# Kernel tuning notes

Measured on AMD Instinct MI355X. Metric: run time of the kernel, lower is better.

The kernel has to match this reference:

```python
import jax, jax.numpy as jnp
import numpy as np

TOP_K = 4  # num_experts_per_tok


def setup_inputs() -> dict:
    key = jax.random.key(0)
    ks = jax.random.split(key, 7)
    B, S, H, E, I = 1, 1024, 1024, 16, 2880
    scale_h = 1.0 / np.sqrt(H)
    scale_i = 1.0 / np.sqrt(I)
    return {
        "hidden_states": jax.random.normal(ks[0], (B, S, H), jnp.float32),
        "gate_w": jax.random.normal(ks[1], (E, H), jnp.float32) * scale_h,
        "gate_b": jax.random.normal(ks[2], (E,), jnp.float32) * 0.01,
        "gate_up_proj": jax.random.normal(ks[3], (E, H, 2 * I), jnp.float32) * scale_h,
        "gate_up_proj_bias": jax.random.normal(ks[4], (E, 2 * I), jnp.float32) * 0.01,
        "down_proj": jax.random.normal(ks[5], (E, I, H), jnp.float32) * scale_i,
        "down_proj_bias": jax.random.normal(ks[6], (E, H), jnp.float32) * 0.01,
    }


def reference(hidden_states, gate_w, gate_b, gate_up_proj, gate_up_proj_bias,
              down_proj, down_proj_bias):
    B, S, H = hidden_states.shape
    E = gate_w.shape[0]
    I = down_proj.shape[1]
    x = hidden_states.reshape(-1, H)  # [T, H]
    T = x.shape[0]

    # Router: top-k logits, softmax over selected logits only
    router_logits = x @ gate_w.T + gate_b          # [T, E]
    top_vals, top_idx = jax.lax.top_k(router_logits, TOP_K)
    routing_weights = jax.nn.softmax(top_vals, axis=-1)  # [T, K]

    # Combine matrix: C[t, e] = routing weight of expert e for token t (0 if unselected)
    C = jnp.zeros((T, E), x.dtype).at[jnp.arange(T)[:, None], top_idx].add(routing_weights)

    # Dense per-expert MLP (reference computes all experts, combine masks unselected)
    gu = jnp.einsum('th,ehf->tef', x, gate_up_proj) + gate_up_proj_bias[None]  # [T, E, 2I]
    gate, up = gu[..., :I], gu[..., I:]
    inter = jax.nn.silu(gate) * up                                            # [T, E, I]
    expert_out = jnp.einsum('tei,eih->teh', inter, down_proj) + down_proj_bias[None]  # [T, E, H]
    out = jnp.einsum('teh,te->th', expert_out, C)                             # [T, H]

    return out.reshape(B, S, H), router_logits
```

## Files before the change

kernel.cpp:

```cpp
#include <hip/hip_runtime.h>
#include <hip/hip_bf16.h>
#include <stdint.h>

#define T_TOK 1024
#define HDIM  1024
#define NEXP  16
#define IDIM  2880
#define GU_COLS (2*IDIM)
#define TOPK  4

using short4v  = __attribute__((ext_vector_type(4))) short;
using short8   = __attribute__((ext_vector_type(8))) short;
using ushort4v = __attribute__((ext_vector_type(4))) unsigned short;
using f32x4    = __attribute__((ext_vector_type(4))) float;

__device__ __forceinline__ unsigned short f2b(float f) {
    union { float f; unsigned u; } x; x.f = f;
    unsigned r = x.u + 0x7FFFu + ((x.u >> 16) & 1u);
    return (unsigned short)(r >> 16);
}

typedef const __attribute__((address_space(1))) unsigned int* gas1_t;
typedef __attribute__((address_space(3))) unsigned int* las3_t;
__device__ __forceinline__ void gload16(const void* g, void* l) {
    __builtin_amdgcn_global_load_lds((gas1_t)g, (las3_t)l, 16, 0, 0);
}

__global__ __launch_bounds__(256) void router_kernel(
    const float* __restrict__ x, const float* __restrict__ gw,
    const float* __restrict__ gb, float* __restrict__ logits_out,
    int* __restrict__ counts, int* __restrict__ lists, float* __restrict__ wts,
    int* __restrict__ tokslot4, float* __restrict__ wts4,
    unsigned short* __restrict__ xb)
{
    int t = blockIdx.x;
    int tid = threadIdx.x;
    const float* xr = x + (size_t)t * HDIM;
    {
        float4 v = *(const float4*)(xr + tid * 4);
        ushort4v b; b.x = f2b(v.x); b.y = f2b(v.y); b.z = f2b(v.z); b.w = f2b(v.w);
        *(ushort4v*)(xb + (size_t)t * HDIM + tid * 4) = b;
    }
    int e = tid >> 4;
    int l16 = tid & 15;
    const float* wr = gw + (size_t)e * HDIM;
    float p = 0.f;
    for (int h = l16; h < HDIM; h += 16) p += xr[h] * wr[h];
    p += __shfl_xor(p, 8);
    p += __shfl_xor(p, 4);
    p += __shfl_xor(p, 2);
    p += __shfl_xor(p, 1);
    __shared__ float sl[NEXP];
    if (l16 == 0) {
        float v = p + gb[e];
        sl[e] = v;
        logits_out[t * NEXP + e] = v;
    }
    __syncthreads();
    if (tid == 0) {
        float v[NEXP];
#pragma unroll
        for (int i = 0; i < NEXP; ++i) v[i] = sl[i];
        int idx[TOPK]; float tv[TOPK];
        unsigned used = 0;
#pragma unroll
        for (int k = 0; k < TOPK; ++k) {
            float best = -__builtin_inff(); int bi = 0;
#pragma unroll
            for (int i = 0; i < NEXP; ++i)
                if (!((used >> i) & 1u) && v[i] > best) { best = v[i]; bi = i; }
            used |= 1u << bi; idx[k] = bi; tv[k] = best;
        }
        float m = tv[0];
        float ex[TOPK], s = 0.f;
#pragma unroll
        for (int k = 0; k < TOPK; ++k) { ex[k] = expf(tv[k] - m); s += ex[k]; }
#pragma unroll
        for (int k = 0; k < TOPK; ++k) {
            float w = ex[k] / s;
            int slot = atomicAdd(&counts[idx[k]], 1);
            lists[idx[k] * T_TOK + slot] = t;
            wts[idx[k] * T_TOK + slot] = w;
            tokslot4[t * TOPK + k] = (idx[k] << 16) | slot;
            wts4[t * TOPK + k] = w;
        }
    }
}

__global__ void offsets_kernel(const int* __restrict__ counts, int* __restrict__ offsets)
{
    if (threadIdx.x == 0) {
        int o = 0;
        for (int e = 0; e < NEXP; ++e) { offsets[e] = o; o += counts[e]; }
        offsets[NEXP] = o;
    }
}

__global__ __launch_bounds__(512) void gu_kernel(
    const unsigned short* __restrict__ xb, const float* __restrict__ gup,
    const float* __restrict__ gub, const int* __restrict__ counts,
    const int* __restrict__ offsets, const int* __restrict__ lists,
    unsigned short* __restrict__ inter)
{
    int bid = blockIdx.x;
    int xcd = bid & 7;
    int r   = bid >> 3;
    int nt  = r % 90;
    int s   = r / 90;
    int e   = xcd + ((s & 1) << 3);
    int mt  = s >> 1;
    int ne = counts[e];
    if (mt * 256 >= ne) return;

    int tid = threadIdx.x;
    int wave = tid >> 6, lane = tid & 63;
    int l16 = lane & 15, lq = lane >> 4;

    __shared__ int tokid[256];
    __shared__ unsigned short As[256 * 64];
    __shared__ unsigned short Bs[64 * 64];

    if (tid < 256) {
        int slot = mt * 256 + tid;
        tokid[tid] = (slot < ne) ? lists[e * T_TOK + slot] : lists[e * T_TOK];
    }
    __syncthreads();

    const float* gup_e = gup + (size_t)e * HDIM * GU_COLS;

    int at = tid - 256;
    const unsigned short* asrc[8];
    if (tid >= 256) {
#pragma unroll
        for (int i = 0; i < 8; ++i) {
            int s2 = at + i * 256;
            int row = s2 >> 3, c = s2 & 7;
            asrc[i] = xb + (size_t)tokid[row] * HDIM + ((c ^ (row & 7)) * 8);
        }
    }
    int nb = tid & 15, kb = tid >> 4;
    const float* bsrc = nullptr;
    if (tid < 256) {
        int n0 = nb * 4;
        size_t col = (n0 < 32) ? (size_t)(nt * 32 + n0) : (size_t)(IDIM + nt * 32 + (n0 - 32));
        bsrc = gup_e + (size_t)(kb * 4) * GU_COLS + col;
    }

    f32x4 acc[2][4];
#pragma unroll
    for (int i = 0; i < 2; ++i)
#pragma unroll
        for (int f = 0; f < 4; ++f) acc[i][f] = (f32x4){0.f, 0.f, 0.f, 0.f};

    float4 br0, br1, br2, br3;
    if (tid < 256) {
        br0 = *(const float4*)(bsrc);
        br1 = *(const float4*)(bsrc + GU_COLS);
        br2 = *(const float4*)(bsrc + 2 * GU_COLS);
        br3 = *(const float4*)(bsrc + 3 * GU_COLS);
    }

    for (int kk = 0; kk < HDIM; kk += 64) {
        __syncthreads();
        if (tid >= 256) {
#pragma unroll
            for (int i = 0; i < 8; ++i)
                gload16(asrc[i] + kk, As + ((size_t)(at + i * 256)) * 8);
        } else {
#pragma unroll
            for (int j = 0; j < 4; ++j) {
                int n = nb * 4 + j;
                int slot = kb ^ (n & 15);
                ushort4v b;
                b.x = f2b((&br0.x)[j]); b.y = f2b((&br1.x)[j]);
                b.z = f2b((&br2.x)[j]); b.w = f2b((&br3.x)[j]);
                *(ushort4v*)&Bs[n * 64 + slot * 4] = b;
            }
        }
        __syncthreads();
        if (tid < 256 && kk + 64 < HDIM) {
            const float* sp = bsrc + (size_t)(kk + 64) * GU_COLS;
            br0 = *(const float4*)(sp);
            br1 = *(const float4*)(sp + GU_COLS);
            br2 = *(const float4*)(sp + 2 * GU_COLS);
            br3 = *(const float4*)(sp + 3 * GU_COLS);
        }
        __builtin_amdgcn_s_setprio(1);
#pragma unroll
        for (int ks = 0; ks < 2; ++ks) {
            short8 a[2], b[4];
#pragma unroll
            for (int i = 0; i < 2; ++i) {
                int row = wave * 32 + i * 16 + l16;
                int q = ks * 4 + lq;
                a[i] = *(const short8*)&As[row * 64 + ((q ^ (row & 7)) * 8)];
            }
#pragma unroll
            for (int f = 0; f < 4; ++f) {
                int n = f * 16 + l16;
                int u0 = (ks * 8 + lq * 2) ^ (n & 15);
                int u1 = (ks * 8 + lq * 2 + 1) ^ (n & 15);
                short4v h0 = *(const short4v*)&Bs[n * 64 + u0 * 4];
                short4v h1 = *(const short4v*)&Bs[n * 64 + u1 * 4];
                b[f] = __builtin_shufflevector(h0, h1, 0, 1, 2, 3, 4, 5, 6, 7);
            }
#pragma unroll
            for (int i = 0; i < 2; ++i)
#pragma unroll
                for (int f = 0; f < 4; ++f)
                    acc[i][f] = __builtin_amdgcn_mfma_f32_16x16x32_bf16(a[i], b[f], acc[i][f], 0, 0, 0);
        }
        __builtin_amdgcn_s_setprio(0);
    }

    int off = offsets[e];
    const float* gbe = gub + (size_t)e * GU_COLS;
#pragma unroll
    for (int j = 0; j < 2; ++j) {
        int col = j * 16 + l16;
        float bg = gbe[nt * 32 + col];
        float bu = gbe[IDIM + nt * 32 + col];
#pragma unroll
        for (int i = 0; i < 2; ++i)
#pragma unroll
            for (int r2 = 0; r2 < 4; ++r2) {
                int row = wave * 32 + i * 16 + lq * 4 + r2;
                int slot = mt * 256 + row;
                if (slot < ne) {
                    float g = acc[i][j][r2] + bg;
                    float u = acc[i][j + 2][r2] + bu;
                    float sg = g / (1.f + expf(-g));
                    inter[(size_t)(off + slot) * IDIM + nt * 32 + col] = f2b(sg * u);
                }
            }
    }
}

__global__ __launch_bounds__(512) void down_kernel(
    const unsigned short* __restrict__ inter, const float* __restrict__ dw,
    const float* __restrict__ db, const int* __restrict__ counts,
    const int* __restrict__ offsets, float* __restrict__ eo)
{
    int bid = blockIdx.x;
    int xcd = bid & 7;
    int r   = bid >> 3;
    int ht  = r & 15;
    int s   = r >> 4;
    int e   = xcd + ((s & 1) << 3);
    int mt  = s >> 1;
    int ne = counts[e];
    if (mt * 256 >= ne) return;

    int tid = threadIdx.x;
    int wave = tid >> 6, lane = tid & 63;
    int l16 = lane & 15, lq = lane >> 4;

    __shared__ unsigned short As[256 * 64];
    __shared__ unsigned short Bs[64 * 64];

    int off = offsets[e];

    const float* dw_e = dw + (size_t)e * IDIM * HDIM;

    int at = tid - 256;
    const unsigned short* asrc[8];
    if (tid >= 256) {
#pragma unroll
        for (int i = 0; i < 8; ++i) {
            int s2 = at + i * 256;
            int row = s2 >> 3, c = s2 & 7;
            int slotr = mt * 256 + row; if (slotr >= ne) slotr = ne - 1;
            asrc[i] = inter + (size_t)(off + slotr) * IDIM + ((c ^ (row & 7)) * 8);
        }
    }
    int nb = tid & 15, kb = tid >> 4;
    const float* bsrc = nullptr;
    if (tid < 256)
        bsrc = dw_e + (size_t)(kb * 4) * HDIM + ht * 64 + nb * 4;

    f32x4 acc[2][4];
#pragma unroll
    for (int i = 0; i < 2; ++i)
#pragma unroll
        for (int f = 0; f < 4; ++f) acc[i][f] = (f32x4){0.f, 0.f, 0.f, 0.f};

    float4 br0, br1, br2, br3;
    if (tid < 256) {
        br0 = *(const float4*)(bsrc);
        br1 = *(const float4*)(bsrc + HDIM);
        br2 = *(const float4*)(bsrc + 2 * HDIM);
        br3 = *(const float4*)(bsrc + 3 * HDIM);
    }

    for (int kk = 0; kk < IDIM; kk += 64) {
        __syncthreads();
        if (tid >= 256) {
#pragma unroll
            for (int i = 0; i < 8; ++i)
                gload16(asrc[i] + kk, As + ((size_t)(at + i * 256)) * 8);
        } else {
#pragma unroll
            for (int j = 0; j < 4; ++j) {
                int n = nb * 4 + j;
                int slot = kb ^ (n & 15);
                ushort4v b;
                b.x = f2b((&br0.x)[j]); b.y = f2b((&br1.x)[j]);
                b.z = f2b((&br2.x)[j]); b.w = f2b((&br3.x)[j]);
                *(ushort4v*)&Bs[n * 64 + slot * 4] = b;
            }
        }
        __syncthreads();
        if (tid < 256 && kk + 64 < IDIM) {
            const float* sp = bsrc + (size_t)(kk + 64) * HDIM;
            br0 = *(const float4*)(sp);
            br1 = *(const float4*)(sp + HDIM);
            br2 = *(const float4*)(sp + 2 * HDIM);
            br3 = *(const float4*)(sp + 3 * HDIM);
        }
        __builtin_amdgcn_s_setprio(1);
#pragma unroll
        for (int ks = 0; ks < 2; ++ks) {
            short8 a[2], b[4];
#pragma unroll
            for (int i = 0; i < 2; ++i) {
                int row = wave * 32 + i * 16 + l16;
                int q = ks * 4 + lq;
                a[i] = *(const short8*)&As[row * 64 + ((q ^ (row & 7)) * 8)];
            }
#pragma unroll
            for (int f = 0; f < 4; ++f) {
                int n = f * 16 + l16;
                int u0 = (ks * 8 + lq * 2) ^ (n & 15);
                int u1 = (ks * 8 + lq * 2 + 1) ^ (n & 15);
                short4v h0 = *(const short4v*)&Bs[n * 64 + u0 * 4];
                short4v h1 = *(const short4v*)&Bs[n * 64 + u1 * 4];
                b[f] = __builtin_shufflevector(h0, h1, 0, 1, 2, 3, 4, 5, 6, 7);
            }
#pragma unroll
            for (int i = 0; i < 2; ++i)
#pragma unroll
                for (int f = 0; f < 4; ++f)
                    acc[i][f] = __builtin_amdgcn_mfma_f32_16x16x32_bf16(a[i], b[f], acc[i][f], 0, 0, 0);
        }
        __builtin_amdgcn_s_setprio(0);
    }

    const float* db_e = db + (size_t)e * HDIM;
#pragma unroll
    for (int f = 0; f < 4; ++f) {
        int h = ht * 64 + f * 16 + l16;
        float bias = db_e[h];
#pragma unroll
        for (int i = 0; i < 2; ++i)
#pragma unroll
            for (int r2 = 0; r2 < 4; ++r2) {
                int row = wave * 32 + i * 16 + lq * 4 + r2;
                int slot = mt * 256 + row;
                if (slot < ne)
                    eo[(size_t)(off + slot) * HDIM + h] = acc[i][f][r2] + bias;
            }
    }
}

__global__ __launch_bounds__(256) void gather_kernel(
    const float* __restrict__ eo, const int* __restrict__ tokslot4,
    const float* __restrict__ wts4, const int* __restrict__ offsets,
    float* __restrict__ out)
{
    int t = blockIdx.x;
    int tid = threadIdx.x;
    int rows[TOPK]; float w[TOPK];
#pragma unroll
    for (int k = 0; k < TOPK; ++k) {
        int ts = tokslot4[t * TOPK + k];
        int e = ts >> 16, slot = ts & 0xFFFF;
        rows[k] = offsets[e] + slot;
        w[k] = wts4[t * TOPK + k];
    }
    int h0 = tid * 4;
    float4 s = make_float4(0.f, 0.f, 0.f, 0.f);
#pragma unroll
    for (int k = 0; k < TOPK; ++k) {
        float4 v = *(const float4*)(eo + (size_t)rows[k] * HDIM + h0);
        s.x += w[k] * v.x; s.y += w[k] * v.y;
        s.z += w[k] * v.z; s.w += w[k] * v.w;
    }
    *(float4*)(out + (size_t)t * HDIM + h0) = s;
}

extern "C" void kernel_launch(void* const* d_in, const int* in_sizes, int n_in,
                              void* d_out, int out_size, void* d_ws, size_t ws_size,
                              hipStream_t stream)
{
    const float* x   = (const float*)d_in[0];
    const float* gw  = (const float*)d_in[1];
    const float* gb  = (const float*)d_in[2];
    const float* gup = (const float*)d_in[3];
    const float* gub = (const float*)d_in[4];
    const float* dw  = (const float*)d_in[5];
    const float* db  = (const float*)d_in[6];

    float* out        = (float*)d_out;
    float* logits_out = out + (size_t)T_TOK * HDIM;

    char* ws = (char*)d_ws;
    int*   counts   = (int*)(ws + 0);
    int*   offsets  = (int*)(ws + 256);
    int*   lists    = (int*)(ws + 512);
    float* wts      = (float*)(ws + 512 + 65536);
    int*   tokslot4 = (int*)(ws + 512 + 131072);
    float* wts4     = (float*)(ws + 512 + 131072 + 16384);
    unsigned short* xb    = (unsigned short*)(ws + 164352);
    unsigned short* inter = (unsigned short*)(ws + 2261504);
    float*          eo    = (float*)(ws + 25854464);

    hipMemsetAsync(counts, 0, 64, stream);

    router_kernel<<<T_TOK, 256, 0, stream>>>(x, gw, gb, logits_out, counts, lists, wts, tokslot4, wts4, xb);
    offsets_kernel<<<1, 64, 0, stream>>>(counts, offsets);
    gu_kernel<<<8 * 90 * 8, 512, 0, stream>>>(xb, gup, gub, counts, offsets, lists, inter);
    down_kernel<<<8 * 16 * 8, 512, 0, stream>>>(inter, dw, db, counts, offsets, eo);
    gather_kernel<<<T_TOK, 256, 0, stream>>>(eo, tokslot4, wts4, offsets, out);
}
```

Before: 303.7 us.

## Double-buffer LDS tiles in gate-up and down GEMMs with async prefetch

```diff
diff --git a/kernel.cpp b/kernel.cpp
--- a/kernel.cpp
+++ b/kernel.cpp
@@ -115,32 +115,28 @@
     int tid = threadIdx.x;
     int wave = tid >> 6, lane = tid & 63;
     int l16 = lane & 15, lq = lane >> 4;
-
-    __shared__ int tokid[256];
-    __shared__ unsigned short As[256 * 64];
-    __shared__ unsigned short Bs[64 * 64];
-
-    if (tid < 256) {
-        int slot = mt * 256 + tid;
-        tokid[tid] = (slot < ne) ? lists[e * T_TOK + slot] : lists[e * T_TOK];
-    }
-    __syncthreads();
+    bool a_wave = (tid >= 256);
+
+    __shared__ unsigned short As[2 * 256 * 64];
+    __shared__ unsigned short Bs[2 * 64 * 64];
 
     const float* gup_e = gup + (size_t)e * HDIM * GU_COLS;
 
     int at = tid - 256;
     const unsigned short* asrc[8];
-    if (tid >= 256) {
+    if (a_wave) {
 #pragma unroll
         for (int i = 0; i < 8; ++i) {
             int s2 = at + i * 256;
             int row = s2 >> 3, c = s2 & 7;
-            asrc[i] = xb + (size_t)tokid[row] * HDIM + ((c ^ (row & 7)) * 8);
+            int slot = mt * 256 + row;
+            int tok = lists[e * T_TOK + (slot < ne ? slot : 0)];
+            asrc[i] = xb + (size_t)tok * HDIM + ((c ^ (row & 7)) * 8);
         }
     }
     int nb = tid & 15, kb = tid >> 4;
     const float* bsrc = nullptr;
-    if (tid < 256) {
+    if (!a_wave) {
         int n0 = nb * 4;
         size_t col = (n0 < 32) ? (size_t)(nt * 32 + n0) : (size_t)(IDIM + nt * 32 + (n0 - 32));
         bsrc = gup_e + (size_t)(kb * 4) * GU_COLS + col;
@@ -153,38 +149,69 @@
         for (int f = 0; f < 4; ++f) acc[i][f] = (f32x4){0.f, 0.f, 0.f, 0.f};
 
     float4 br0, br1, br2, br3;
-    if (tid < 256) {
+    if (a_wave) {
+#pragma unroll
+        for (int i = 0; i < 8; ++i)
+            gload16(asrc[i], As + ((size_t)(at + i * 256)) * 8);
+    } else {
         br0 = *(const float4*)(bsrc);
         br1 = *(const float4*)(bsrc + GU_COLS);
         br2 = *(const float4*)(bsrc + 2 * GU_COLS);
         br3 = *(const float4*)(bsrc + 3 * GU_COLS);
-    }
-
-    for (int kk = 0; kk < HDIM; kk += 64) {
-        __syncthreads();
-        if (tid >= 256) {
-#pragma unroll
-            for (int i = 0; i < 8; ++i)
-                gload16(asrc[i] + kk, As + ((size_t)(at + i * 256)) * 8);
+#pragma unroll
+        for (int j = 0; j < 4; ++j) {
+            int n = nb * 4 + j;
+            int slot = kb ^ (n & 15);
+            ushort4v b;
+            b.x = f2b((&br0.x)[j]); b.y = f2b((&br1.x)[j]);
+            b.z = f2b((&br2.x)[j]); b.w = f2b((&br3.x)[j]);
+            *(ushort4v*)&Bs[n * 64 + slot * 4] = b;
+        }
+        const float* sp = bsrc + (size_t)64 * GU_COLS;
+        br0 = *(const float4*)(sp);
+        br1 = *(const float4*)(sp + GU_COLS);
+        br2 = *(const float4*)(sp + 2 * GU_COLS);
+        br3 = *(const float4*)(sp + 3 * GU_COLS);
+    }
+    __syncthreads();
+
+    const int NP = HDIM / 64;
+    for (int p = 0; p < NP; ++p) {
+        int cur = p & 1, nxt = cur ^ 1;
+        __builtin_amdgcn_s_barrier();
+        __builtin_amdgcn_sched_barrier(0);
+        if (p + 1 < NP) {
+            if (a_wave) {
+#pragma unroll
+                for (int i = 0; i < 8; ++i)
+                    gload16(asrc[i] + (p + 1) * 64, As + (size_t)nxt * 16384 + ((size_t)(at + i * 256)) * 8);
+            } else {
+#pragma unroll
+                for (int j = 0; j < 4; ++j) {
+                    int n = nb * 4 + j;
+                    int slot = kb ^ (n & 15);
+                    ushort4v b;
+                    b.x = f2b((&br0.x)[j]); b.y = f2b((&br1.x)[j]);
+                    b.z = f2b((&br2.x)[j]); b.w = f2b((&br3.x)[j]);
+                    *(ushort4v*)&Bs[nxt * 4096 + n * 64 + slot * 4] = b;
+                }
+                if (p + 2 < NP) {
+                    const float* sp = bsrc + (size_t)(p + 2) * 64 * GU_COLS;
+                    br0 = *(const float4*)(sp);
+                    br1 = *(const float4*)(sp + GU_COLS);
+                    br2 = *(const float4*)(sp + 2 * GU_COLS);
+                    br3 = *(const float4*)(sp + 3 * GU_COLS);
+                }
+            }
+        }
+        if (a_wave) {
+            if (p + 1 < NP) asm volatile("s_waitcnt vmcnt(8)" ::: "memory");
+            else            asm volatile("s_waitcnt vmcnt(0)" ::: "memory");
         } else {
-#pragma unroll
-            for (int j = 0; j < 4; ++j) {
-                int n = nb * 4 + j;
-                int slot = kb ^ (n & 15);
-                ushort4v b;
-                b.x = f2b((&br0.x)[j]); b.y = f2b((&br1.x)[j]);
-                b.z = f2b((&br2.x)[j]); b.w = f2b((&br3.x)[j]);
-                *(ushort4v*)&Bs[n * 64 + slot * 4] = b;
-            }
-        }
-        __syncthreads();
-        if (tid < 256 && kk + 64 < HDIM) {
-            const float* sp = bsrc + (size_t)(kk + 64) * GU_COLS;
-            br0 = *(const float4*)(sp);
-            br1 = *(const float4*)(sp + GU_COLS);
-            br2 = *(const float4*)(sp + 2 * GU_COLS);
-            br3 = *(const float4*)(sp + 3 * GU_COLS);
-        }
+            asm volatile("s_waitcnt lgkmcnt(0)" ::: "memory");
+        }
+        __builtin_amdgcn_s_barrier();
+        __builtin_amdgcn_sched_barrier(0);
         __builtin_amdgcn_s_setprio(1);
 #pragma unroll
         for (int ks = 0; ks < 2; ++ks) {
@@ -193,15 +220,15 @@
             for (int i = 0; i < 2; ++i) {
                 int row = wave * 32 + i * 16 + l16;
                 int q = ks * 4 + lq;
-                a[i] = *(const short8*)&As[row * 64 + ((q ^ (row & 7)) * 8)];
+                a[i] = *(const short8*)&As[cur * 16384 + row * 64 + ((q ^ (row & 7)) * 8)];
             }
 #pragma unroll
             for (int f = 0; f < 4; ++f) {
                 int n = f * 16 + l16;
                 int u0 = (ks * 8 + lq * 2) ^ (n & 15);
                 int u1 = (ks * 8 + lq * 2 + 1) ^ (n & 15);
-                short4v h0 = *(const short4v*)&Bs[n * 64 + u0 * 4];
-                short4v h1 = *(const short4v*)&Bs[n * 64 + u1 * 4];
+                short4v h0 = *(const short4v*)&Bs[cur * 4096 + n * 64 + u0 * 4];
+                short4v h1 = *(const short4v*)&Bs[cur * 4096 + n * 64 + u1 * 4];
                 b[f] = __builtin_shufflevector(h0, h1, 0, 1, 2, 3, 4, 5, 6, 7);
             }
 #pragma unroll
@@ -254,17 +281,17 @@
     int tid = threadIdx.x;
     int wave = tid >> 6, lane = tid & 63;
     int l16 = lane & 15, lq = lane >> 4;
-
-    __shared__ unsigned short As[256 * 64];
-    __shared__ unsigned short Bs[64 * 64];
+    bool a_wave = (tid >= 256);
+
+    __shared__ unsigned short As[2 * 256 * 64];
+    __shared__ unsigned short Bs[2 * 64 * 64];
 
     int off = offsets[e];
-
     const float* dw_e = dw + (size_t)e * IDIM * HDIM;
 
     int at = tid - 256;
     const unsigned short* asrc[8];
-    if (tid >= 256) {
+    if (a_wave) {
 #pragma unroll
         for (int i = 0; i < 8; ++i) {
             int s2 = at + i * 256;
@@ -275,7 +302,7 @@
     }
     int nb = tid & 15, kb = tid >> 4;
     const float* bsrc = nullptr;
-    if (tid < 256)
+    if (!a_wave)
         bsrc = dw_e + (size_t)(kb * 4) * HDIM + ht * 64 + nb * 4;
 
     f32x4 acc[2][4];
@@ -285,38 +312,69 @@
         for (int f = 0; f < 4; ++f) acc[i][f] = (f32x4){0.f, 0.f, 0.f, 0.f};
 
     float4 br0, br1, br2, br3;
-    if (tid < 256) {
+    if (a_wave) {
+#pragma unroll
+        for (int i = 0; i < 8; ++i)
+            gload16(asrc[i], As + ((size_t)(at + i * 256)) * 8);
+    } else {
         br0 = *(const float4*)(bsrc);
         br1 = *(const float4*)(bsrc + HDIM);
         br2 = *(const float4*)(bsrc + 2 * HDIM);
         br3 = *(const float4*)(bsrc + 3 * HDIM);
-    }
-
-    for (int kk = 0; kk < IDIM; kk += 64) {
-        __syncthreads();
-        if (tid >= 256) {
-#pragma unroll
-            for (int i = 0; i < 8; ++i)
-                gload16(asrc[i] + kk, As + ((size_t)(at + i * 256)) * 8);
+#pragma unroll
+        for (int j = 0; j < 4; ++j) {
+            int n = nb * 4 + j;
+            int slot = kb ^ (n & 15);
+            ushort4v b;
+            b.x = f2b((&br0.x)[j]); b.y = f2b((&br1.x)[j]);
+            b.z = f2b((&br2.x)[j]); b.w = f2b((&br3.x)[j]);
+            *(ushort4v*)&Bs[n * 64 + slot * 4] = b;
+        }
+        const float* sp = bsrc + (size_t)64 * HDIM;
+        br0 = *(const float4*)(sp);
+        br1 = *(const float4*)(sp + HDIM);
+        br2 = *(const float4*)(sp + 2 * HDIM);
+        br3 = *(const float4*)(sp + 3 * HDIM);
+    }
+    __syncthreads();
+
+    const int NP = IDIM / 64;
+    for (int p = 0; p < NP; ++p) {
+        int cur = p & 1, nxt = cur ^ 1;
+        __builtin_amdgcn_s_barrier();
+        __builtin_amdgcn_sched_barrier(0);
+        if (p + 1 < NP) {
+            if (a_wave) {
+#pragma unroll
+                for (int i = 0; i < 8; ++i)
+                    gload16(asrc[i] + (p + 1) * 64, As + (size_t)nxt * 16384 + ((size_t)(at + i * 256)) * 8);
+            } else {
+#pragma unroll
+                for (int j = 0; j < 4; ++j) {
+                    int n = nb * 4 + j;
+                    int slot = kb ^ (n & 15);
+                    ushort4v b;
+                    b.x = f2b((&br0.x)[j]); b.y = f2b((&br1.x)[j]);
+                    b.z = f2b((&br2.x)[j]); b.w = f2b((&br3.x)[j]);
+                    *(ushort4v*)&Bs[nxt * 4096 + n * 64 + slot * 4] = b;
+                }
+                if (p + 2 < NP) {
+                    const float* sp = bsrc + (size_t)(p + 2) * 64 * HDIM;
+                    br0 = *(const float4*)(sp);
+                    br1 = *(const float4*)(sp + HDIM);
+                    br2 = *(const float4*)(sp + 2 * HDIM);
+                    br3 = *(const float4*)(sp + 3 * HDIM);
+                }
+            }
+        }
+        if (a_wave) {
+            if (p + 1 < NP) asm volatile("s_waitcnt vmcnt(8)" ::: "memory");
+            else            asm volatile("s_waitcnt vmcnt(0)" ::: "memory");
         } else {
-#pragma unroll
-            for (int j = 0; j < 4; ++j) {
-                int n = nb * 4 + j;
-                int slot = kb ^ (n & 15);
-                ushort4v b;
-                b.x = f2b((&br0.x)[j]); b.y = f2b((&br1.x)[j]);
-                b.z = f2b((&br2.x)[j]); b.w = f2b((&br3.x)[j]);
-                *(ushort4v*)&Bs[n * 64 + slot * 4] = b;
-            }
-        }
-        __syncthreads();
-        if (tid < 256 && kk + 64 < IDIM) {
-            const float* sp = bsrc + (size_t)(kk + 64) * HDIM;
-            br0 = *(const float4*)(sp);
-            br1 = *(const float4*)(sp + HDIM);
-            br2 = *(const float4*)(sp + 2 * HDIM);
-            br3 = *(const float4*)(sp + 3 * HDIM);
-        }
+            asm volatile("s_waitcnt lgkmcnt(0)" ::: "memory");
+        }
+        __builtin_amdgcn_s_barrier();
+        __builtin_amdgcn_sched_barrier(0);
         __builtin_amdgcn_s_setprio(1);
 #pragma unroll
         for (int ks = 0; ks < 2; ++ks) {
@@ -325,15 +383,15 @@
             for (int i = 0; i < 2; ++i) {
                 int row = wave * 32 + i * 16 + l16;
                 int q = ks * 4 + lq;
-                a[i] = *(const short8*)&As[row * 64 + ((q ^ (row & 7)) * 8)];
+                a[i] = *(const short8*)&As[cur * 16384 + row * 64 + ((q ^ (row & 7)) * 8)];
             }
 #pragma unroll
             for (int f = 0; f < 4; ++f) {
                 int n = f * 16 + l16;
                 int u0 = (ks * 8 + lq * 2) ^ (n & 15);
                 int u1 = (ks * 8 + lq * 2 + 1) ^ (n & 15);
-                short4v h0 = *(const short4v*)&Bs[n * 64 + u0 * 4];
-                short4v h1 = *(const short4v*)&Bs[n * 64 + u1 * 4];
+                short4v h0 = *(const short4v*)&Bs[cur * 4096 + n * 64 + u0 * 4];
+                short4v h1 = *(const short4v*)&Bs[cur * 4096 + n * 64 + u1 * 4];
                 b[f] = __builtin_shufflevector(h0, h1, 0, 1, 2, 3, 4, 5, 6, 7);
             }
 #pragma unroll
```

After: 388.4 us. 1.28x slower.

## Split down-projection K dimension across two blocks and sum partials in gather

Applied to the files above, without the earlier changes.

```diff
diff --git a/kernel.cpp b/kernel.cpp
--- a/kernel.cpp
+++ b/kernel.cpp
@@ -8,6 +8,7 @@
 #define IDIM  2880
 #define GU_COLS (2*IDIM)
 #define TOPK  4
+#define ESTRIDE ((size_t)T_TOK * TOPK * HDIM)
 
 using short4v  = __attribute__((ext_vector_type(4))) short;
 using short8   = __attribute__((ext_vector_type(8))) short;
@@ -245,12 +246,17 @@
     int xcd = bid & 7;
     int r   = bid >> 3;
     int ht  = r & 15;
-    int s   = r >> 4;
+    int s2  = r >> 4;
+    int ksp = s2 & 1;
+    int s   = s2 >> 1;
     int e   = xcd + ((s & 1) << 3);
     int mt  = s >> 1;
     int ne = counts[e];
     if (mt * 256 >= ne) return;
 
+    int k0   = ksp * 1472;
+    int kend = ksp ? IDIM : 1472;
+
     int tid = threadIdx.x;
     int wave = tid >> 6, lane = tid & 63;
     int l16 = lane & 15, lq = lane >> 4;
@@ -259,16 +265,16 @@
     __shared__ unsigned short Bs[64 * 64];
 
     int off = offsets[e];
-
     const float* dw_e = dw + (size_t)e * IDIM * HDIM;
+    float* eo_k = eo + (size_t)ksp * ESTRIDE;
 
     int at = tid - 256;
     const unsigned short* asrc[8];
     if (tid >= 256) {
 #pragma unroll
         for (int i = 0; i < 8; ++i) {
-            int s2 = at + i * 256;
-            int row = s2 >> 3, c = s2 & 7;
+            int s3 = at + i * 256;
+            int row = s3 >> 3, c = s3 & 7;
             int slotr = mt * 256 + row; if (slotr >= ne) slotr = ne - 1;
             asrc[i] = inter + (size_t)(off + slotr) * IDIM + ((c ^ (row & 7)) * 8);
         }
@@ -286,13 +292,14 @@
 
     float4 br0, br1, br2, br3;
     if (tid < 256) {
-        br0 = *(const float4*)(bsrc);
-        br1 = *(const float4*)(bsrc + HDIM);
-        br2 = *(const float4*)(bsrc + 2 * HDIM);
-        br3 = *(const float4*)(bsrc + 3 * HDIM);
-    }
-
-    for (int kk = 0; kk < IDIM; kk += 64) {
+        const float* sp = bsrc + (size_t)k0 * HDIM;
+        br0 = *(const float4*)(sp);
+        br1 = *(const float4*)(sp + HDIM);
+        br2 = *(const float4*)(sp + 2 * HDIM);
+        br3 = *(const float4*)(sp + 3 * HDIM);
+    }
+
+    for (int kk = k0; kk < kend; kk += 64) {
         __syncthreads();
         if (tid >= 256) {
 #pragma unroll
@@ -310,7 +317,7 @@
             }
         }
         __syncthreads();
-        if (tid < 256 && kk + 64 < IDIM) {
+        if (tid < 256 && kk + 64 < kend) {
             const float* sp = bsrc + (size_t)(kk + 64) * HDIM;
             br0 = *(const float4*)(sp);
             br1 = *(const float4*)(sp + HDIM);
@@ -349,7 +356,7 @@
 #pragma unroll
     for (int f = 0; f < 4; ++f) {
         int h = ht * 64 + f * 16 + l16;
-        float bias = db_e[h];
+        float bias = (ksp == 0) ? db_e[h] : 0.f;
 #pragma unroll
         for (int i = 0; i < 2; ++i)
 #pragma unroll
@@ -357,7 +364,7 @@
                 int row = wave * 32 + i * 16 + lq * 4 + r2;
                 int slot = mt * 256 + row;
                 if (slot < ne)
-                    eo[(size_t)(off + slot) * HDIM + h] = acc[i][f][r2] + bias;
+                    eo_k[(size_t)(off + slot) * HDIM + h] = acc[i][f][r2] + bias;
             }
     }
 }
@@ -381,9 +388,10 @@
     float4 s = make_float4(0.f, 0.f, 0.f, 0.f);
 #pragma unroll
     for (int k = 0; k < TOPK; ++k) {
-        float4 v = *(const float4*)(eo + (size_t)rows[k] * HDIM + h0);
-        s.x += w[k] * v.x; s.y += w[k] * v.y;
-        s.z += w[k] * v.z; s.w += w[k] * v.w;
+        float4 v0 = *(const float4*)(eo + (size_t)rows[k] * HDIM + h0);
+        float4 v1 = *(const float4*)(eo + ESTRIDE + (size_t)rows[k] * HDIM + h0);
+        s.x += w[k] * (v0.x + v1.x); s.y += w[k] * (v0.y + v1.y);
+        s.z += w[k] * (v0.z + v1.z); s.w += w[k] * (v0.w + v1.w);
     }
     *(float4*)(out + (size_t)t * HDIM + h0) = s;
 }
@@ -419,6 +427,6 @@
     router_kernel<<<T_TOK, 256, 0, stream>>>(x, gw, gb, logits_out, counts, lists, wts, tokslot4, wts4, xb);
     offsets_kernel<<<1, 64, 0, stream>>>(counts, offsets);
     gu_kernel<<<8 * 90 * 8, 512, 0, stream>>>(xb, gup, gub, counts, offsets, lists, inter);
-    down_kernel<<<8 * 16 * 8, 512, 0, stream>>>(inter, dw, db, counts, offsets, eo);
+    down_kernel<<<2 * 8 * 16 * 8, 512, 0, stream>>>(inter, dw, db, counts, offsets, eo);
     gather_kernel<<<T_TOK, 256, 0, stream>>>(eo, tokslot4, wts4, offsets, out);
 }
```

Result: slower. 320.6 us (+5.6%).
